# Kernel tuning notes

Measured on AMD Instinct MI355X. Metric: run time of the kernel, lower is better.

Reference implementation:

```python
import jax, jax.numpy as jnp
import numpy as np

N = 16384
E = 262144
IN_F, HID, ENC = 3, 128, 768
NEG_SLOPE = 0.2
EPS = 1e-5


def _glorot(key, shape):
    lim = float(np.sqrt(6.0 / (shape[0] + shape[1])))
    return jax.random.uniform(key, shape, jnp.float32, -lim, lim)


def layernorm(x, g, b):
    mu = jnp.mean(x, axis=-1, keepdims=True)
    var = jnp.mean(jnp.square(x - mu), axis=-1, keepdims=True)
    return (x - mu) * jax.lax.rsqrt(var + EPS) * g + b


def gatv2(x, src, dst, Wl, bl, Wr, br, att, bias, n_nodes):
    # single-head GATv2: message = lin_l(x)[src], score from lin_l(x)[src] + lin_r(x)[dst]
    xl = x @ Wl + bl                                  # [N, C]
    xr = x @ Wr + br                                  # [N, C]
    e = jax.nn.leaky_relu(xl[src] + xr[dst], NEG_SLOPE) @ att   # [E]
    m = jax.ops.segment_max(e, dst, num_segments=n_nodes)       # per-dst max (self-loops => no empty segs)
    ex = jnp.exp(e - m[dst])
    denom = jax.ops.segment_sum(ex, dst, num_segments=n_nodes)
    alpha = ex / denom[dst]                           # [E]
    out = jax.ops.segment_sum(alpha[:, None] * xl[src], dst, num_segments=n_nodes)
    return out + bias


def setup_inputs() -> dict:
    key = jax.random.key(0)
    ks = jax.random.split(key, 12)
    x = jax.random.normal(ks[0], (N, IN_F), jnp.float32)
    edge_index = jax.random.randint(ks[1], (2, E), 0, N, jnp.int64)
    return {
        "x": x,
        "edge_index": edge_index,
        "Wfc": _glorot(ks[2], (IN_F, ENC)),
        "bfc": jnp.zeros((ENC,), jnp.float32),
        "W1l": _glorot(ks[3], (IN_F, HID)),
        "b1l": jnp.zeros((HID,), jnp.float32),
        "W1r": _glorot(ks[4], (IN_F, HID)),
        "b1r": jnp.zeros((HID,), jnp.float32),
        "att1": _glorot(ks[5], (HID, 1))[:, 0],
        "bias1": jnp.zeros((HID,), jnp.float32),
        "g_bn1": jnp.ones((HID,), jnp.float32),
        "bb_bn1": jnp.zeros((HID,), jnp.float32),
        "W2l": _glorot(ks[6], (HID, ENC)),
        "b2l": jnp.zeros((ENC,), jnp.float32),
        "W2r": _glorot(ks[7], (HID, ENC)),
        "b2r": jnp.zeros((ENC,), jnp.float32),
        "att2": _glorot(ks[8], (ENC, 1))[:, 0],
        "bias2": jnp.zeros((ENC,), jnp.float32),
        "g_norm": jnp.ones((ENC,), jnp.float32),
        "b_norm": jnp.zeros((ENC,), jnp.float32),
    }


def reference(x, edge_index, Wfc, bfc, W1l, b1l, W1r, b1r, att1, bias1,
              g_bn1, bb_bn1, W2l, b2l, W2r, b2r, att2, bias2, g_norm, b_norm):
    loops = jnp.arange(N, dtype=edge_index.dtype)
    src = jnp.concatenate([edge_index[0], loops])   # add self-loops (PyG default)
    dst = jnp.concatenate([edge_index[1], loops])
    res = x @ Wfc + bfc                              # [N, ENC]
    h = gatv2(x, src, dst, W1l, b1l, W1r, b1r, att1, bias1, N)
    h = jax.nn.elu(layernorm(h, g_bn1, bb_bn1))
    h = gatv2(h, src, dst, W2l, b2l, W2r, b2r, att2, bias2, N)
    return layernorm(h + res, g_norm, b_norm)
```

## Files before the change

kernel.cpp:

```cpp
#include <hip/hip_runtime.h>

#define N_NODES 16384
#define N_EDGES 262144
#define EP (N_EDGES + N_NODES)
#define HID 128
#define ENC 768
#define EPSV 1e-5f

typedef unsigned short u16;
typedef unsigned char u8;
using f32x4  = __attribute__((ext_vector_type(4))) float;
using bf16x8 = __attribute__((ext_vector_type(8))) short;
using v2f    = __attribute__((ext_vector_type(2))) float;

__device__ __forceinline__ float wave_sum(float v){
  #pragma unroll
  for(int m=32;m>=1;m>>=1) v += __shfl_xor(v, m, 64);
  return v;
}
__device__ __forceinline__ unsigned bf16rtne(float f){
  const unsigned u = __float_as_uint(f);
  return (u + 0x7fffu + ((u>>16)&1u)) >> 16;
}
__device__ __forceinline__ unsigned pack2(float a, float b){
  return bf16rtne(a) | (bf16rtne(b) << 16);
}
__device__ __forceinline__ float bf2f(u16 h){ return __uint_as_float(((unsigned)h) << 16); }
__device__ __forceinline__ float plo(unsigned u){ return __uint_as_float(u << 16); }
__device__ __forceinline__ float phi(unsigned u){ return __uint_as_float(u & 0xffff0000u); }
__device__ __forceinline__ u8 f2fp8(float v){
  return (u8)(__builtin_amdgcn_cvt_pk_fp8_f32(v, v, 0, false) & 0xff);
}

#define QD(ax, j, q) { \
  const v2f f01 = __builtin_amdgcn_cvt_pk_f32_fp8(ax, false); \
  const v2f f23 = __builtin_amdgcn_cvt_pk_f32_fp8(ax, true);  \
  q = fmaf(sg[j],   __builtin_fabsf(f01.x+xr[j]),   q); \
  q = fmaf(sg[j+1], __builtin_fabsf(f01.y+xr[j+1]), q); \
  q = fmaf(sg[j+2], __builtin_fabsf(f23.x+xr[j+2]), q); \
  q = fmaf(sg[j+3], __builtin_fabsf(f23.y+xr[j+3]), q); }

#define LIN1_BLKS (N_NODES/4)
#define WPREP_BLKS (2*ENC*HID/256)
#define HIST_BLKS (EP/256)
#define W2A_BLKS 258
__global__ __launch_bounds__(256) void prep_kernel(
    const float* __restrict__ x,
    const float* __restrict__ W1l, const float* __restrict__ b1l,
    const float* __restrict__ W1r, const float* __restrict__ b1r,
    const float* __restrict__ att1,
    const float* __restrict__ W2l, const float* __restrict__ W2r,
    const float* __restrict__ b2l, const float* __restrict__ b2r,
    const float* __restrict__ att2,
    const int* __restrict__ ei,
    unsigned* __restrict__ xl1u, unsigned* __restrict__ xr1u,
    float* __restrict__ dotl1, float* __restrict__ dotr1,
    u16* __restrict__ Wtb, float* __restrict__ w2a,
    int* __restrict__ hist){
  const int bid = blockIdx.x;
  if(bid < LIN1_BLKS){
    const int lane = threadIdx.x & 63;
    const int n = bid*4 + (threadIdx.x >> 6);
    const float x0 = x[n*3], x1 = x[n*3+1], x2 = x[n*3+2];
    const int c0 = 2*lane, c1 = 2*lane + 1;
    const float la = x0*W1l[c0] + x1*W1l[HID+c0] + x2*W1l[2*HID+c0] + b1l[c0];
    const float lb = x0*W1l[c1] + x1*W1l[HID+c1] + x2*W1l[2*HID+c1] + b1l[c1];
    const float ra = x0*W1r[c0] + x1*W1r[HID+c0] + x2*W1r[2*HID+c0] + b1r[c0];
    const float rb = x0*W1r[c1] + x1*W1r[HID+c1] + x2*W1r[2*HID+c1] + b1r[c1];
    const float aa = att1[c0], ab = att1[c1];
    const float dl = wave_sum(la*aa + lb*ab);
    const float dr = wave_sum(ra*aa + rb*ab);
    if(lane == 0){ dotl1[n] = 0.6f*dl; dotr1[n] = 0.6f*dr; }
    xl1u[n*64+lane] = pack2(la, lb);
    xr1u[n*64+lane] = pack2(ra, rb);
  } else if(bid < LIN1_BLKS + WPREP_BLKS){
    const int idx = (bid - LIN1_BLKS)*256 + threadIdx.x;
    const int n = idx >> 7, k = idx & 127;
    const float v = (n < ENC) ? W2l[k*ENC + n] : W2r[k*ENC + (n-ENC)];
    Wtb[idx] = (u16)bf16rtne(v);
  } else if(bid < LIN1_BLKS + WPREP_BLKS + HIST_BLKS){
    const int i = (bid - LIN1_BLKS - WPREP_BLKS)*256 + threadIdx.x;
    const int dst = (i < N_EDGES) ? ei[N_EDGES + i] : (i - N_EDGES);
    atomicAdd(&hist[dst], 1);
  } else {
    const int idx = bid - (LIN1_BLKS + WPREP_BLKS + HIST_BLKS);
    const float* src = (idx < 128) ? (W2l + (size_t)idx*ENC)
                     : (idx < 256) ? (W2r + (size_t)(idx-128)*ENC)
                     : (idx == 256) ? b2l : b2r;
    float partial = 0.f;
    for(int c = threadIdx.x; c < ENC; c += 256) partial += src[c]*att2[c];
    partial = wave_sum(partial);
    __shared__ float red4[4];
    if((threadIdx.x & 63) == 0) red4[threadIdx.x >> 6] = partial;
    __syncthreads();
    if(threadIdx.x == 0) w2a[idx] = red4[0]+red4[1]+red4[2]+red4[3];
  }
}

__global__ __launch_bounds__(1024) void scan_kernel(
    const int* __restrict__ hist, int* __restrict__ rowstart){
  __shared__ int sums[1024];
  const int t = threadIdx.x;
  const int base = t*16;
  int loc[16];
  int s = 0;
  #pragma unroll
  for(int i=0;i<16;i++){ loc[i] = s; s += hist[base+i]; }
  sums[t] = s;
  __syncthreads();
  for(int off=1; off<1024; off<<=1){
    int v = 0;
    if(t >= off) v = sums[t-off];
    __syncthreads();
    if(t >= off) sums[t] += v;
    __syncthreads();
  }
  const int prev = (t==0) ? 0 : sums[t-1];
  #pragma unroll
  for(int i=0;i<16;i++) rowstart[base+i] = prev + loc[i];
  if(t == 1023) rowstart[N_NODES] = EP;
}

__global__ __launch_bounds__(256) void scatter_kernel(
    const int* __restrict__ ei, const int* __restrict__ rowstart,
    int* __restrict__ hist, int* __restrict__ ssrc){
  const int i = blockIdx.x*256 + threadIdx.x;
  const int src = (i < N_EDGES) ? ei[i]           : (i - N_EDGES);
  const int dst = (i < N_EDGES) ? ei[N_EDGES + i] : (i - N_EDGES);
  const int idx = atomicSub(&hist[dst], 1) - 1;
  ssrc[rowstart[dst] + idx] = src;
}

__global__ __launch_bounds__(256) void node1_kernel(
    const unsigned* __restrict__ xl1u, const unsigned* __restrict__ xr1u,
    const float* __restrict__ att1,
    const float* __restrict__ dotl1, const float* __restrict__ dotr1,
    const float* __restrict__ bias1,
    const float* __restrict__ g1, const float* __restrict__ b1,
    const float* __restrict__ w2a,
    const int* __restrict__ rowstart, const int* __restrict__ ssrc,
    unsigned* __restrict__ h1u,
    float* __restrict__ dotl2, float* __restrict__ dotr2){
  const int lane = threadIdx.x & 63;
  const int n = blockIdx.x*4 + (threadIdx.x >> 6);
  const int g = lane >> 4, k = lane & 15;
  float xr[8], sa[8];
  {
    const uint4 u = *(const uint4*)(xr1u + n*64 + 4*k);
    xr[0]=plo(u.x); xr[1]=phi(u.x); xr[2]=plo(u.y); xr[3]=phi(u.y);
    xr[4]=plo(u.z); xr[5]=phi(u.z); xr[6]=plo(u.w); xr[7]=phi(u.w);
    const float4 a0 = *(const float4*)(att1 + 8*k);
    const float4 a1 = *(const float4*)(att1 + 8*k + 4);
    sa[0]=0.4f*a0.x; sa[1]=0.4f*a0.y; sa[2]=0.4f*a0.z; sa[3]=0.4f*a0.w;
    sa[4]=0.4f*a1.x; sa[5]=0.4f*a1.y; sa[6]=0.4f*a1.z; sa[7]=0.4f*a1.w;
  }
  const float ebase = dotr1[n];
  float acc[8] = {0,0,0,0,0,0,0,0};
  float denom = 0.f;
  const int p0 = rowstart[n], p1 = rowstart[n+1];
  int base = p0;
  for(; base + 8 <= p1; base += 8){
    const int iA = base + g, iB = base + 4 + g;
    const int sA = ssrc[iA], sB = ssrc[iB];
    const uint4 uA = *(const uint4*)(xl1u + sA*64 + 4*k);
    const uint4 uB = *(const uint4*)(xl1u + sB*64 + 4*k);
    const float dlA = dotl1[sA], dlB = dotl1[sB];
    float a[8], b[8];
    a[0]=plo(uA.x); a[1]=phi(uA.x); a[2]=plo(uA.y); a[3]=phi(uA.y);
    a[4]=plo(uA.z); a[5]=phi(uA.z); a[6]=plo(uA.w); a[7]=phi(uA.w);
    b[0]=plo(uB.x); b[1]=phi(uB.x); b[2]=plo(uB.y); b[3]=phi(uB.y);
    b[4]=plo(uB.z); b[5]=phi(uB.z); b[6]=plo(uB.w); b[7]=phi(uB.w);
    float qA = 0.f, qB = 0.f;
    #pragma unroll
    for(int j=0;j<8;j++){
      qA = fmaf(sa[j], __builtin_fabsf(a[j]+xr[j]), qA);
      qB = fmaf(sa[j], __builtin_fabsf(b[j]+xr[j]), qB);
    }
    #pragma unroll
    for(int m=1;m<16;m<<=1){
      qA += __shfl_xor(qA, m, 64);
      qB += __shfl_xor(qB, m, 64);
    }
    const float wA = __expf(qA + dlA + ebase);
    const float wB = __expf(qB + dlB + ebase);
    denom += wA + wB;
    #pragma unroll
    for(int j=0;j<8;j++) acc[j] = fmaf(wA, a[j], fmaf(wB, b[j], acc[j]));
  }
  for(; base < p1; base += 4){
    const int idx = base + g;
    const bool valid = idx < p1;
    const int s = ssrc[valid ? idx : (p1-1)];
    const uint4 u = *(const uint4*)(xl1u + s*64 + 4*k);
    float a[8];
    a[0]=plo(u.x); a[1]=phi(u.x); a[2]=plo(u.y); a[3]=phi(u.y);
    a[4]=plo(u.z); a[5]=phi(u.z); a[6]=plo(u.w); a[7]=phi(u.w);
    const float dlv = dotl1[s];
    float q = 0.f;
    #pragma unroll
    for(int j=0;j<8;j++) q = fmaf(sa[j], __builtin_fabsf(a[j]+xr[j]), q);
    q += __shfl_xor(q, 1, 64);
    q += __shfl_xor(q, 2, 64);
    q += __shfl_xor(q, 4, 64);
    q += __shfl_xor(q, 8, 64);
    float w = __expf(q + dlv + ebase);
    w = valid ? w : 0.f;
    denom += w;
    #pragma unroll
    for(int j=0;j<8;j++) acc[j] = fmaf(w, a[j], acc[j]);
  }
  #pragma unroll
  for(int m=16; m<64; m<<=1){
    denom += __shfl_xor(denom, m, 64);
    #pragma unroll
    for(int j=0;j<8;j++) acc[j] += __shfl_xor(acc[j], m, 64);
  }
  const float inv = 1.f/denom;
  const float4 bb0 = *(const float4*)(bias1 + 8*k);
  const float4 bb1 = *(const float4*)(bias1 + 8*k + 4);
  float y[8];
  y[0]=acc[0]*inv+bb0.x; y[1]=acc[1]*inv+bb0.y; y[2]=acc[2]*inv+bb0.z; y[3]=acc[3]*inv+bb0.w;
  y[4]=acc[4]*inv+bb1.x; y[5]=acc[5]*inv+bb1.y; y[6]=acc[6]*inv+bb1.z; y[7]=acc[7]*inv+bb1.w;
  float ls = 0.f, lq = 0.f;
  #pragma unroll
  for(int j=0;j<8;j++){ ls += y[j]; lq += y[j]*y[j]; }
  ls = wave_sum(ls); lq = wave_sum(lq);
  const float mu  = ls * (1.f/(4*HID));
  const float var = lq * (1.f/(4*HID)) - mu*mu;
  const float r = rsqrtf(var + EPSV);
  const float4 gg0 = *(const float4*)(g1 + 8*k);
  const float4 gg1 = *(const float4*)(g1 + 8*k + 4);
  const float4 ob0 = *(const float4*)(b1 + 8*k);
  const float4 ob1 = *(const float4*)(b1 + 8*k + 4);
  const float gv[8] = {gg0.x,gg0.y,gg0.z,gg0.w,gg1.x,gg1.y,gg1.z,gg1.w};
  const float bv[8] = {ob0.x,ob0.y,ob0.z,ob0.w,ob1.x,ob1.y,ob1.z,ob1.w};
  float z[8];
  #pragma unroll
  for(int j=0;j<8;j++){
    float zz = (y[j]-mu)*r*gv[j] + bv[j];
    z[j] = zz > 0.f ? zz : expm1f(zz);
  }
  float dl2 = 0.f, dr2 = 0.f;
  #pragma unroll
  for(int j=0;j<8;j++){
    dl2 = fmaf(z[j], w2a[8*k+j], dl2);
    dr2 = fmaf(z[j], w2a[128+8*k+j], dr2);
  }
  dl2 = wave_sum(dl2); dr2 = wave_sum(dr2);
  if(lane == 0){
    dotl2[n] = 0.6f*(0.25f*dl2 + w2a[256]);
    dotr2[n] = 0.6f*(0.25f*dr2 + w2a[257]);
  }
  if(g == 0){
    uint4 o;
    o.x = pack2(z[0], z[1]); o.y = pack2(z[2], z[3]);
    o.z = pack2(z[4], z[5]); o.w = pack2(z[6], z[7]);
    *(uint4*)(h1u + n*64 + 4*k) = o;
  }
}

#define LBM 128
#define LBN 128
__global__ __launch_bounds__(256) void mfma_lin2_kernel(
    const u16* __restrict__ h1b, const u16* __restrict__ Wtb,
    const float* __restrict__ b2l, const float* __restrict__ b2r,
    u8* __restrict__ xl8, u16* __restrict__ xr2u){
  __shared__ __align__(16) u16 Cs[LBM*128];
  const int t = threadIdx.x;
  const int mb = blockIdx.x * LBM;
  const int nb = blockIdx.y * LBN;
  const int w = t >> 6, lane = t & 63;
  const int l15 = lane & 15, g = lane >> 4;
  const int ar0 = mb + w*32 + l15, ar1 = ar0 + 16;
  bf16x8 a0[4], a1[4];
  #pragma unroll
  for(int ks=0;ks<4;ks++){
    a0[ks] = *(const bf16x8*)(h1b + (size_t)ar0*128 + ks*32 + g*8);
    a1[ks] = *(const bf16x8*)(h1b + (size_t)ar1*128 + ks*32 + g*8);
  }
  f32x4 acc0[8], acc1[8];
  #pragma unroll
  for(int j=0;j<8;j++){ acc0[j]=(f32x4){0,0,0,0}; acc1[j]=(f32x4){0,0,0,0}; }
  #pragma unroll
  for(int j=0;j<8;j++){
    const int brn = nb + j*16 + l15;
    #pragma unroll
    for(int ks=0;ks<4;ks++){
      const bf16x8 b = *(const bf16x8*)(Wtb + (size_t)brn*128 + ks*32 + g*8);
      acc0[j] = __builtin_amdgcn_mfma_f32_16x16x32_bf16(a0[ks], b, acc0[j], 0,0,0);
      acc1[j] = __builtin_amdgcn_mfma_f32_16x16x32_bf16(a1[ks], b, acc1[j], 0,0,0);
    }
  }
  if(nb < ENC){
    u8* Cs8 = (u8*)Cs;
    float biasj[8];
    #pragma unroll
    for(int j=0;j<8;j++) biasj[j] = b2l[nb + j*16 + l15];
    #pragma unroll
    for(int j=0;j<8;j++){
      const int col = j*16 + l15;
      #pragma unroll
      for(int r4=0;r4<4;r4++){
        const int row0 = w*32 + g*4 + r4;
        Cs8[row0*128 + (col ^ ((row0&7)<<4))] = f2fp8(acc0[j][r4] + biasj[j]);
        const int row1 = row0 + 16;
        Cs8[row1*128 + (col ^ ((row1&7)<<4))] = f2fp8(acc1[j][r4] + biasj[j]);
      }
    }
    __syncthreads();
    #pragma unroll
    for(int idx=t; idx<LBM*8; idx+=256){
      const int row = idx >> 3, ch = idx & 7;
      const uint4 v = *(const uint4*)(Cs8 + row*128 + ((ch*16) ^ ((row&7)<<4)));
      *(uint4*)(xl8 + (size_t)(mb+row)*ENC + nb + ch*16) = v;
    }
  } else {
    const float* bsrc = b2r + (nb - ENC);
    float biasj[8];
    #pragma unroll
    for(int j=0;j<8;j++) biasj[j] = bsrc[j*16 + l15];
    #pragma unroll
    for(int j=0;j<8;j++){
      const int coll = j*16 + l15;
      #pragma unroll
      for(int r4=0;r4<4;r4++){
        const int row0 = w*32 + g*4 + r4;
        *(u16*)((char*)Cs + row0*256 + ((coll*2) ^ ((row0&7)<<4))) =
            (u16)bf16rtne(acc0[j][r4] + biasj[j]);
        const int row1 = row0 + 16;
        *(u16*)((char*)Cs + row1*256 + ((coll*2) ^ ((row1&7)<<4))) =
            (u16)bf16rtne(acc1[j][r4] + biasj[j]);
      }
    }
    __syncthreads();
    u16* dst0 = xr2u + (nb - ENC);
    const int rr = t >> 4, cc = t & 15;
    #pragma unroll
    for(int it=0; it<8; ++it){
      const int row = it*16 + rr;
      const uint4 v = *(const uint4*)((const char*)Cs + row*256 + ((cc*16) ^ ((row&7)<<4)));
      *(uint4*)(dst0 + (size_t)(mb+row)*ENC + cc*8) = v;
    }
  }
}

__global__ __launch_bounds__(256) void node2b_kernel(
    const u8* __restrict__ xl8, const u8* __restrict__ xr2u8,
    const float* __restrict__ att2,
    const float* __restrict__ dotl2, const float* __restrict__ dotr2,
    const unsigned* __restrict__ h1u,
    const int* __restrict__ rowstart, const int* __restrict__ ssrc,
    unsigned* __restrict__ aggb){
  const int lane = threadIdx.x & 63;
  const int n = blockIdx.x*4 + (threadIdx.x >> 6);
  float sg[12], xr[12];
  {
    const float4* A4 = (const float4*)(att2 + lane*12);
    const float4 s0 = A4[0], s1 = A4[1], s2 = A4[2];
    sg[0]=0.4f*s0.x; sg[1]=0.4f*s0.y; sg[2]=0.4f*s0.z; sg[3]=0.4f*s0.w;
    sg[4]=0.4f*s1.x; sg[5]=0.4f*s1.y; sg[6]=0.4f*s1.z; sg[7]=0.4f*s1.w;
    sg[8]=0.4f*s2.x; sg[9]=0.4f*s2.y; sg[10]=0.4f*s2.z; sg[11]=0.4f*s2.w;
    const u8* xrrow = xr2u8 + (size_t)n*(ENC*2) + lane*24;
    const uint2 r0 = *(const uint2*)(xrrow);
    const uint2 r1 = *(const uint2*)(xrrow + 8);
    const uint2 r2 = *(const uint2*)(xrrow + 16);
    xr[0]=plo(r0.x); xr[1]=phi(r0.x); xr[2]=plo(r0.y); xr[3]=phi(r0.y);
    xr[4]=plo(r1.x); xr[5]=phi(r1.x); xr[6]=plo(r1.y); xr[7]=phi(r1.y);
    xr[8]=plo(r2.x); xr[9]=phi(r2.x); xr[10]=plo(r2.y); xr[11]=phi(r2.y);
  }
  const float ebase = dotr2[n];
  float denom = 0.f, acc0 = 0.f, acc1 = 0.f;
  int p = rowstart[n];
  const int p1 = rowstart[n+1];
  for(; p+7 < p1; p += 8){
    int s[8];
    #pragma unroll
    for(int e=0;e<8;e++) s[e] = ssrc[p+e];
    uint3 a[8]; unsigned h[8]; float dl[8];
    #pragma unroll
    for(int e=0;e<8;e++){
      a[e]  = *(const uint3*)(xl8 + (size_t)s[e]*ENC + lane*12);
      h[e]  = h1u[s[e]*64 + lane];
      dl[e] = dotl2[s[e]];
    }
    float q[8];
    #pragma unroll
    for(int e=0;e<8;e++){
      q[e] = 0.f;
      QD(a[e].x, 0, q[e]) QD(a[e].y, 4, q[e]) QD(a[e].z, 8, q[e])
    }
    #pragma unroll
    for(int m=32;m>=1;m>>=1){
      #pragma unroll
      for(int e=0;e<8;e++) q[e] += __shfl_xor(q[e], m, 64);
    }
    #pragma unroll
    for(int e=0;e<8;e++){
      const float w = __expf(q[e] + dl[e] + ebase);
      denom += w;
      acc0 += w*plo(h[e]);
      acc1 += w*phi(h[e]);
    }
  }
  for(; p < p1; ++p){
    const int s0 = ssrc[p];
    const uint3 a0 = *(const uint3*)(xl8 + (size_t)s0*ENC + lane*12);
    float q0 = 0.f;
    QD(a0.x, 0, q0) QD(a0.y, 4, q0) QD(a0.z, 8, q0)
    const unsigned h0 = h1u[s0*64 + lane];
    const float w0 = __expf(wave_sum(q0) + dotl2[s0] + ebase);
    denom += w0; acc0 += w0*plo(h0); acc1 += w0*phi(h0);
  }
  const float inv = 1.f/denom;
  aggb[n*64 + lane] = pack2(acc0*inv, acc1*inv);
}

#define YSTR 770
__global__ __launch_bounds__(256) void gemm3_mfma_kernel(
    const u16* __restrict__ aggb, const u16* __restrict__ Wtb,
    const float* __restrict__ b2l, const float* __restrict__ bias2,
    const float* __restrict__ x, const float* __restrict__ Wfc,
    const float* __restrict__ bfc,
    const float* __restrict__ gn, const float* __restrict__ bn,
    float* __restrict__ out){
  __shared__ u16 Ys[64*YSTR];
  __shared__ float cbs[ENC];
  __shared__ float wfs[3][ENC];
  __shared__ float mus[64], rss[64];
  const int t = threadIdx.x;
  const int mb = blockIdx.x * 64;
  for(int c=t; c<ENC; c+=256){
    cbs[c] = b2l[c] + bias2[c] + bfc[c];
    wfs[0][c] = Wfc[c]; wfs[1][c] = Wfc[ENC+c]; wfs[2][c] = Wfc[2*ENC+c];
  }
  const int w = t >> 6, lane = t & 63;
  const int l15 = lane & 15, g = lane >> 4;
  const int ar = mb + w*16 + l15;
  bf16x8 a[4];
  #pragma unroll
  for(int ks=0;ks<4;ks++)
    a[ks] = *(const bf16x8*)(aggb + (size_t)ar*128 + ks*32 + g*8);
  float xv0[4], xv1[4], xv2[4];
  #pragma unroll
  for(int r4=0;r4<4;r4++){
    const int rrow = mb + w*16 + g*4 + r4;
    xv0[r4] = x[rrow*3]; xv1[r4] = x[rrow*3+1]; xv2[r4] = x[rrow*3+2];
  }
  float rs[4] = {0,0,0,0}, rq[4] = {0,0,0,0};
  __syncthreads();
  #pragma unroll
  for(int sub=0; sub<6; ++sub){
    const int nb = sub*128;
    f32x4 acc[8];
    #pragma unroll
    for(int j=0;j<8;j++) acc[j]=(f32x4){0,0,0,0};
    #pragma unroll
    for(int j=0;j<8;j++){
      const int brn = nb + j*16 + l15;
      #pragma unroll
      for(int ks=0;ks<4;ks++){
        const bf16x8 b = *(const bf16x8*)(Wtb + (size_t)brn*128 + ks*32 + g*8);
        acc[j] = __builtin_amdgcn_mfma_f32_16x16x32_bf16(a[ks], b, acc[j], 0,0,0);
      }
    }
    #pragma unroll
    for(int j=0;j<8;j++){
      const int col = nb + j*16 + l15;
      const float cb = cbs[col];
      const float w0 = wfs[0][col], w1 = wfs[1][col], w2 = wfs[2][col];
      #pragma unroll
      for(int r4=0;r4<4;r4++){
        const int lrow = w*16 + g*4 + r4;
        const float y = acc[j][r4] + cb + xv0[r4]*w0 + xv1[r4]*w1 + xv2[r4]*w2;
        rs[r4] += y; rq[r4] += y*y;
        Ys[lrow*YSTR + col] = (u16)bf16rtne(y);
      }
    }
  }
  #pragma unroll
  for(int m=8;m>=1;m>>=1){
    #pragma unroll
    for(int r4=0;r4<4;r4++){
      rs[r4] += __shfl_xor(rs[r4], m, 64);
      rq[r4] += __shfl_xor(rq[r4], m, 64);
    }
  }
  if(l15 == 0){
    #pragma unroll
    for(int r4=0;r4<4;r4++){
      const int lrow = w*16 + g*4 + r4;
      const float mu = rs[r4] * (1.f/ENC);
      const float var = rq[r4] * (1.f/ENC) - mu*mu;
      mus[lrow] = mu;
      rss[lrow] = rsqrtf(var + EPSV);
    }
  }
  __syncthreads();
  float gv[12], bv[12];
  #pragma unroll
  for(int j2=0;j2<12;j2++){ gv[j2] = gn[lane + j2*64]; bv[j2] = bn[lane + j2*64]; }
  for(int r=0; r<16; ++r){
    const int lrow = w*16 + r;
    const float mu = mus[lrow], rstd = rss[lrow];
    float* orow = out + (size_t)(mb+lrow)*ENC;
    #pragma unroll
    for(int j2=0;j2<12;j2++){
      const float y = bf2f(Ys[lrow*YSTR + lane + j2*64]);
      orow[lane + j2*64] = (y - mu)*rstd*gv[j2] + bv[j2];
    }
  }
}

extern "C" void kernel_launch(void* const* d_in, const int* in_sizes, int n_in,
                              void* d_out, int out_size, void* d_ws, size_t ws_size,
                              hipStream_t stream) {
  const float* x    = (const float*)d_in[0];
  const int*   ei   = (const int*)  d_in[1];
  const float* Wfc  = (const float*)d_in[2];
  const float* bfc  = (const float*)d_in[3];
  const float* W1l  = (const float*)d_in[4];
  const float* b1l  = (const float*)d_in[5];
  const float* W1r  = (const float*)d_in[6];
  const float* b1r  = (const float*)d_in[7];
  const float* att1 = (const float*)d_in[8];
  const float* bias1= (const float*)d_in[9];
  const float* g1   = (const float*)d_in[10];
  const float* bb1  = (const float*)d_in[11];
  const float* W2l  = (const float*)d_in[12];
  const float* b2l  = (const float*)d_in[13];
  const float* W2r  = (const float*)d_in[14];
  const float* b2r  = (const float*)d_in[15];
  const float* att2 = (const float*)d_in[16];
  const float* bias2= (const float*)d_in[17];
  const float* gn   = (const float*)d_in[18];
  const float* bn   = (const float*)d_in[19];
  float* out = (float*)d_out;

  char* w = (char*)d_ws;
  auto alloc = [&](size_t bytes){ void* p = (void*)w; w += (bytes + 255) & ~(size_t)255; return p; };
  int*      hist     = (int*)     alloc((size_t)N_NODES*4);
  int*      rowstart = (int*)     alloc((size_t)(N_NODES+1)*4);
  int*      ssrc     = (int*)     alloc((size_t)EP*4);
  unsigned* xl1u     = (unsigned*)alloc((size_t)N_NODES*64*4);
  unsigned* xr1u     = (unsigned*)alloc((size_t)N_NODES*64*4);
  float*    dotl1    = (float*)   alloc((size_t)N_NODES*4);
  float*    dotr1    = (float*)   alloc((size_t)N_NODES*4);
  float*    dotl2    = (float*)   alloc((size_t)N_NODES*4);
  float*    dotr2    = (float*)   alloc((size_t)N_NODES*4);
  unsigned* h1u      = (unsigned*)alloc((size_t)N_NODES*64*4);
  unsigned* aggb     = (unsigned*)alloc((size_t)N_NODES*64*4);
  u8*       xl8      = (u8*)      alloc((size_t)N_NODES*ENC);
  u16*      xr2u     = (u16*)     alloc((size_t)N_NODES*ENC*2);
  u16*      Wtb      = (u16*)     alloc((size_t)2*ENC*HID*2);
  float*    w2a      = (float*)   alloc((size_t)W2A_BLKS*4);

  hipMemsetAsync(hist, 0, (size_t)N_NODES*4, stream);

  prep_kernel<<<LIN1_BLKS+WPREP_BLKS+HIST_BLKS+W2A_BLKS, 256, 0, stream>>>(
      x, W1l, b1l, W1r, b1r, att1, W2l, W2r, b2l, b2r, att2, ei,
      xl1u, xr1u, dotl1, dotr1, Wtb, w2a, hist);
  scan_kernel<<<1, 1024, 0, stream>>>(hist, rowstart);
  scatter_kernel<<<EP/256, 256, 0, stream>>>(ei, rowstart, hist, ssrc);
  node1_kernel<<<N_NODES/4, 256, 0, stream>>>(xl1u, xr1u, att1, dotl1, dotr1,
                                              bias1, g1, bb1, w2a,
                                              rowstart, ssrc, h1u, dotl2, dotr2);
  mfma_lin2_kernel<<<dim3(N_NODES/LBM, 2*ENC/LBN), 256, 0, stream>>>(
      (const u16*)h1u, Wtb, b2l, b2r, xl8, xr2u);
  node2b_kernel<<<N_NODES/4, 256, 0, stream>>>(xl8, (const u8*)xr2u, att2,
                                               dotl2, dotr2, h1u,
                                               rowstart, ssrc, aggb);
  gemm3_mfma_kernel<<<N_NODES/64, 256, 0, stream>>>((const u16*)aggb, Wtb, b2l, bias2,
                                                    x, Wfc, bfc, gn, bn, out);
}
```

Baseline: 186.3 us.

## Split each wave into four 16-lane edge groups in layer-2 aggregation

The layer-2 edge aggregation kernel now splits each wave into four 16-lane groups, each handling a different edge with 16-byte loads of the fp8 xl row. Score reductions shrink to 4 shuffle steps, and a cross-group reduction runs once at the end. The aim is to cut per-edge shuffle overhead and use wider, more efficient memory loads. In exchange each lane holds 48 att and 48 xr values in registers, which raises register pressure (launch bounds ask for 3 blocks). The tail loop also does wasted work on masked edges.

```diff
diff --git a/kernel.cpp b/kernel.cpp
--- a/kernel.cpp
+++ b/kernel.cpp
@@ -39,6 +39,7 @@
   q = fmaf(sg[j+1], __builtin_fabsf(f01.y+xr[j+1]), q); \
   q = fmaf(sg[j+2], __builtin_fabsf(f23.x+xr[j+2]), q); \
   q = fmaf(sg[j+3], __builtin_fabsf(f23.y+xr[j+3]), q); }
+#define QX(u4, j0, q) { QD(u4.x, j0, q) QD(u4.y, (j0)+4, q) QD(u4.z, (j0)+8, q) QD(u4.w, (j0)+12, q) }
 
 #define LIN1_BLKS (N_NODES/4)
 #define WPREP_BLKS (2*ENC*HID/256)
@@ -344,8 +345,8 @@
   }
 }
 
-__global__ __launch_bounds__(256) void node2b_kernel(
-    const u8* __restrict__ xl8, const u8* __restrict__ xr2u8,
+__global__ __launch_bounds__(256, 3) void node2g_kernel(
+    const u8* __restrict__ xl8, const u16* __restrict__ xr2u,
     const float* __restrict__ att2,
     const float* __restrict__ dotl2, const float* __restrict__ dotr2,
     const unsigned* __restrict__ h1u,
@@ -353,66 +354,101 @@
     unsigned* __restrict__ aggb){
   const int lane = threadIdx.x & 63;
   const int n = blockIdx.x*4 + (threadIdx.x >> 6);
-  float sg[12], xr[12];
-  {
-    const float4* A4 = (const float4*)(att2 + lane*12);
-    const float4 s0 = A4[0], s1 = A4[1], s2 = A4[2];
-    sg[0]=0.4f*s0.x; sg[1]=0.4f*s0.y; sg[2]=0.4f*s0.z; sg[3]=0.4f*s0.w;
-    sg[4]=0.4f*s1.x; sg[5]=0.4f*s1.y; sg[6]=0.4f*s1.z; sg[7]=0.4f*s1.w;
-    sg[8]=0.4f*s2.x; sg[9]=0.4f*s2.y; sg[10]=0.4f*s2.z; sg[11]=0.4f*s2.w;
-    const u8* xrrow = xr2u8 + (size_t)n*(ENC*2) + lane*24;
-    const uint2 r0 = *(const uint2*)(xrrow);
-    const uint2 r1 = *(const uint2*)(xrrow + 8);
-    const uint2 r2 = *(const uint2*)(xrrow + 16);
-    xr[0]=plo(r0.x); xr[1]=phi(r0.x); xr[2]=plo(r0.y); xr[3]=phi(r0.y);
-    xr[4]=plo(r1.x); xr[5]=phi(r1.x); xr[6]=plo(r1.y); xr[7]=phi(r1.y);
-    xr[8]=plo(r2.x); xr[9]=phi(r2.x); xr[10]=plo(r2.y); xr[11]=phi(r2.y);
+  const int g = lane >> 4, k = lane & 15;
+  float sg[48], xr[48];
+  #pragma unroll
+  for(int j=0;j<3;j++){
+    const int base = 256*j + 16*k;
+    #pragma unroll
+    for(int b4=0;b4<4;b4++){
+      const float4 s4 = *(const float4*)(att2 + base + 4*b4);
+      sg[16*j+4*b4]   = 0.4f*s4.x; sg[16*j+4*b4+1] = 0.4f*s4.y;
+      sg[16*j+4*b4+2] = 0.4f*s4.z; sg[16*j+4*b4+3] = 0.4f*s4.w;
+    }
+    const uint4 r0 = *(const uint4*)(xr2u + (size_t)n*ENC + base);
+    const uint4 r1 = *(const uint4*)(xr2u + (size_t)n*ENC + base + 8);
+    xr[16*j]   =plo(r0.x); xr[16*j+1] =phi(r0.x); xr[16*j+2] =plo(r0.y); xr[16*j+3] =phi(r0.y);
+    xr[16*j+4] =plo(r0.z); xr[16*j+5] =phi(r0.z); xr[16*j+6] =plo(r0.w); xr[16*j+7] =phi(r0.w);
+    xr[16*j+8] =plo(r1.x); xr[16*j+9] =phi(r1.x); xr[16*j+10]=plo(r1.y); xr[16*j+11]=phi(r1.y);
+    xr[16*j+12]=plo(r1.z); xr[16*j+13]=phi(r1.z); xr[16*j+14]=plo(r1.w); xr[16*j+15]=phi(r1.w);
   }
   const float ebase = dotr2[n];
-  float denom = 0.f, acc0 = 0.f, acc1 = 0.f;
-  int p = rowstart[n];
-  const int p1 = rowstart[n+1];
-  for(; p+7 < p1; p += 8){
-    int s[8];
-    #pragma unroll
-    for(int e=0;e<8;e++) s[e] = ssrc[p+e];
-    uint3 a[8]; unsigned h[8]; float dl[8];
-    #pragma unroll
-    for(int e=0;e<8;e++){
-      a[e]  = *(const uint3*)(xl8 + (size_t)s[e]*ENC + lane*12);
-      h[e]  = h1u[s[e]*64 + lane];
-      dl[e] = dotl2[s[e]];
-    }
-    float q[8];
-    #pragma unroll
-    for(int e=0;e<8;e++){
-      q[e] = 0.f;
-      QD(a[e].x, 0, q[e]) QD(a[e].y, 4, q[e]) QD(a[e].z, 8, q[e])
-    }
-    #pragma unroll
-    for(int m=32;m>=1;m>>=1){
-      #pragma unroll
-      for(int e=0;e<8;e++) q[e] += __shfl_xor(q[e], m, 64);
-    }
-    #pragma unroll
-    for(int e=0;e<8;e++){
-      const float w = __expf(q[e] + dl[e] + ebase);
-      denom += w;
-      acc0 += w*plo(h[e]);
-      acc1 += w*phi(h[e]);
-    }
-  }
-  for(; p < p1; ++p){
-    const int s0 = ssrc[p];
-    const uint3 a0 = *(const uint3*)(xl8 + (size_t)s0*ENC + lane*12);
-    float q0 = 0.f;
-    QD(a0.x, 0, q0) QD(a0.y, 4, q0) QD(a0.z, 8, q0)
-    const unsigned h0 = h1u[s0*64 + lane];
-    const float w0 = __expf(wave_sum(q0) + dotl2[s0] + ebase);
-    denom += w0; acc0 += w0*plo(h0); acc1 += w0*phi(h0);
-  }
-  const float inv = 1.f/denom;
-  aggb[n*64 + lane] = pack2(acc0*inv, acc1*inv);
+  float acc[8] = {0,0,0,0,0,0,0,0};
+  float denom = 0.f;
+  const int p0 = rowstart[n], p1 = rowstart[n+1];
+  int p = p0;
+  for(; p + 8 <= p1; p += 8){
+    const int sA = ssrc[p + g], sB = ssrc[p + 4 + g];
+    const u8* rA = xl8 + (size_t)sA*ENC + 16*k;
+    const u8* rB = xl8 + (size_t)sB*ENC + 16*k;
+    const uint4 a0 = *(const uint4*)(rA);
+    const uint4 a1 = *(const uint4*)(rA + 256);
+    const uint4 a2 = *(const uint4*)(rA + 512);
+    const uint4 b0 = *(const uint4*)(rB);
+    const uint4 b1 = *(const uint4*)(rB + 256);
+    const uint4 b2 = *(const uint4*)(rB + 512);
+    const uint4 hA = *(const uint4*)(h1u + sA*64 + 4*k);
+    const uint4 hB = *(const uint4*)(h1u + sB*64 + 4*k);
+    const float dlA = dotl2[sA], dlB = dotl2[sB];
+    float qA = 0.f, qB = 0.f;
+    QX(a0, 0, qA) QX(a1, 16, qA) QX(a2, 32, qA)
+    QX(b0, 0, qB) QX(b1, 16, qB) QX(b2, 32, qB)
+    #pragma unroll
+    for(int m=1;m<16;m<<=1){
+      qA += __shfl_xor(qA, m, 64);
+      qB += __shfl_xor(qB, m, 64);
+    }
+    const float wA = __expf(qA + dlA + ebase);
+    const float wB = __expf(qB + dlB + ebase);
+    denom += wA + wB;
+    acc[0] += wA*plo(hA.x) + wB*plo(hB.x);
+    acc[1] += wA*phi(hA.x) + wB*phi(hB.x);
+    acc[2] += wA*plo(hA.y) + wB*plo(hB.y);
+    acc[3] += wA*phi(hA.y) + wB*phi(hB.y);
+    acc[4] += wA*plo(hA.z) + wB*plo(hB.z);
+    acc[5] += wA*phi(hA.z) + wB*phi(hB.z);
+    acc[6] += wA*plo(hA.w) + wB*plo(hB.w);
+    acc[7] += wA*phi(hA.w) + wB*phi(hB.w);
+  }
+  for(; p < p1; p += 4){
+    const int idx = p + g;
+    const bool valid = idx < p1;
+    const int s = ssrc[valid ? idx : (p1-1)];
+    const u8* r = xl8 + (size_t)s*ENC + 16*k;
+    const uint4 a0 = *(const uint4*)(r);
+    const uint4 a1 = *(const uint4*)(r + 256);
+    const uint4 a2 = *(const uint4*)(r + 512);
+    const uint4 h = *(const uint4*)(h1u + s*64 + 4*k);
+    const float dlv = dotl2[s];
+    float q = 0.f;
+    QX(a0, 0, q) QX(a1, 16, q) QX(a2, 32, q)
+    q += __shfl_xor(q, 1, 64);
+    q += __shfl_xor(q, 2, 64);
+    q += __shfl_xor(q, 4, 64);
+    q += __shfl_xor(q, 8, 64);
+    float w = __expf(q + dlv + ebase);
+    w = valid ? w : 0.f;
+    denom += w;
+    acc[0] += w*plo(h.x); acc[1] += w*phi(h.x);
+    acc[2] += w*plo(h.y); acc[3] += w*phi(h.y);
+    acc[4] += w*plo(h.z); acc[5] += w*phi(h.z);
+    acc[6] += w*plo(h.w); acc[7] += w*phi(h.w);
+  }
+  #pragma unroll
+  for(int m=16; m<64; m<<=1){
+    denom += __shfl_xor(denom, m, 64);
+    #pragma unroll
+    for(int j=0;j<8;j++) acc[j] += __shfl_xor(acc[j], m, 64);
+  }
+  if(g == 0){
+    const float inv = 1.f/denom;
+    uint4 o;
+    o.x = pack2(acc[0]*inv, acc[1]*inv);
+    o.y = pack2(acc[2]*inv, acc[3]*inv);
+    o.z = pack2(acc[4]*inv, acc[5]*inv);
+    o.w = pack2(acc[6]*inv, acc[7]*inv);
+    *(uint4*)(aggb + n*64 + 4*k) = o;
+  }
 }
 
 #define YSTR 770
@@ -566,7 +602,7 @@
                                               rowstart, ssrc, h1u, dotl2, dotr2);
   mfma_lin2_kernel<<<dim3(N_NODES/LBM, 2*ENC/LBN), 256, 0, stream>>>(
       (const u16*)h1u, Wtb, b2l, b2r, xl8, xr2u);
-  node2b_kernel<<<N_NODES/4, 256, 0, stream>>>(xl8, (const u8*)xr2u, att2,
+  node2g_kernel<<<N_NODES/4, 256, 0, stream>>>(xl8, xr2u, att2,
                                                dotl2, dotr2, h1u,
                                                rowstart, ssrc, aggb);
   gemm3_mfma_kernel<<<N_NODES/64, 256, 0, stream>>>((const u16*)aggb, Wtb, b2l, bias2,
```

New measurement: 189.5 us. Within noise of the previous version (+1.7%).
